# Kernel optimization log

Measured on AMD Instinct MI355X. Metric: run time of the kernel, lower is better.

The kernel has to match this reference:

```python
import jax, jax.numpy as jnp
import numpy as np

N_GROUP = 8
N_ITER = 3


def setup_inputs() -> dict:
    key = jax.random.key(0)
    x = jax.random.normal(key, (16, 64, 64, 512), dtype=jnp.float32)
    return {"x": x}


def reference(x):
    # x: [B, H, W, G*C] NHWC feature map
    B, H, W, Cg = x.shape
    G = N_GROUP
    C = Cg // G
    xr = x.reshape(B, H, W, G, C)  # [B,H,W,G,C]
    # routing logits per (batch, group); broadcastable against xr
    beta = jnp.zeros((B, 1, 1, G, 1), dtype=x.dtype)
    v = jnp.zeros((B, H, W, 1, C), dtype=x.dtype)
    for i in range(N_ITER):
        alpha = jax.nn.sigmoid(beta)                      # [B,1,1,G,1]
        v = jnp.sum(alpha * xr, axis=-2, keepdims=True)   # [B,H,W,1,C]
        if i < N_ITER - 1:
            # agreement: reduce over spatial dims and channels -> per (batch, group)
            beta = beta + jnp.sum(v * xr, axis=(1, 2, 4), keepdims=True)
    return v[..., 0, :]  # [B,H,W,C]
```

## Files before the change

### kernel.cpp

```cpp
#include <hip/hip_runtime.h>
#include <math.h>

#define BATCH   16
#define HW      4096
#define CG      512
#define NPAIR   36
#define F4_PER_POS   128
#define F4_PER_GROUP 16
#define SLOTS_PER_B  65536
#define XB_F4        524288

__global__ __launch_bounds__(256) void gram_kernel(const float* __restrict__ xf,
                                                   float* __restrict__ S) {
    const float4* x = (const float4*)xf;
    const int b = blockIdx.y;
    const int stride = gridDim.x * 256;
    int t = blockIdx.x * 256 + threadIdx.x;

    float acc[NPAIR];
#pragma unroll
    for (int p = 0; p < NPAIR; ++p) acc[p] = 0.f;

    const float4* xb = x + (long)b * XB_F4;
    for (int slot = t; slot < SLOTS_PER_B; slot += stride) {
        const int pos = slot >> 4;
        const int c4  = slot & 15;
        const float4* ptr = xb + pos * F4_PER_POS + c4;
        float4 xg[8];
#pragma unroll
        for (int g = 0; g < 8; ++g) xg[g] = ptr[g * F4_PER_GROUP];
        int p = 0;
#pragma unroll
        for (int g = 0; g < 8; ++g) {
#pragma unroll
            for (int gp = g; gp < 8; ++gp, ++p) {
                acc[p] += xg[g].x * xg[gp].x + xg[g].y * xg[gp].y +
                          xg[g].z * xg[gp].z + xg[g].w * xg[gp].w;
            }
        }
    }

#pragma unroll
    for (int p = 0; p < NPAIR; ++p) {
        float v = acc[p];
#pragma unroll
        for (int off = 32; off; off >>= 1) v += __shfl_xor(v, off, 64);
        acc[p] = v;
    }

    __shared__ float red[4][NPAIR];
    const int lane = threadIdx.x & 63;
    const int wave = threadIdx.x >> 6;
    if (lane == 0) {
#pragma unroll
        for (int p = 0; p < NPAIR; ++p) red[wave][p] = acc[p];
    }
    __syncthreads();
    if (threadIdx.x < NPAIR) {
        float v = red[0][threadIdx.x] + red[1][threadIdx.x] +
                  red[2][threadIdx.x] + red[3][threadIdx.x];
        atomicAdd(&S[b * NPAIR + threadIdx.x], v);
    }
}

__global__ __launch_bounds__(256) void out_kernel(const float* __restrict__ xf,
                                                  const float* __restrict__ S,
                                                  float* __restrict__ outf) {
    const float4* x = (const float4*)xf;
    float4* out = (float4*)outf;
    const int b   = blockIdx.x >> 8;
    const int blk = blockIdx.x & 255;

    __shared__ float alpha1s[8];
    __shared__ float alpha2s[8];

    const int g = threadIdx.x;
    float row[8];
    float beta1 = 0.f;
    if (g < 8) {
#pragma unroll
        for (int gp = 0; gp < 8; ++gp) {
            const int a  = g < gp ? g : gp;
            const int bb = g < gp ? gp : g;
            const int idx = a * 8 - (a * (a - 1)) / 2 + (bb - a);
            row[gp] = S[b * NPAIR + idx];
            beta1 += row[gp];
        }
        beta1 *= 0.5f;
        alpha1s[g] = 1.f / (1.f + expf(-beta1));
    }
    __syncthreads();
    if (g < 8) {
        float beta2 = beta1;
#pragma unroll
        for (int gp = 0; gp < 8; ++gp) beta2 += alpha1s[gp] * row[gp];
        alpha2s[g] = 1.f / (1.f + expf(-beta2));
    }
    __syncthreads();

    float a[8];
#pragma unroll
    for (int gg = 0; gg < 8; ++gg) a[gg] = alpha2s[gg];

    const int t   = blk * 256 + threadIdx.x;
    const int pos = t >> 4;
    const int c4  = t & 15;
    const float4* ptr = x + (long)b * XB_F4 + pos * F4_PER_POS + c4;

    float4 accv = make_float4(0.f, 0.f, 0.f, 0.f);
#pragma unroll
    for (int gg = 0; gg < 8; ++gg) {
        const float4 v = ptr[gg * F4_PER_GROUP];
        accv.x += a[gg] * v.x;
        accv.y += a[gg] * v.y;
        accv.z += a[gg] * v.z;
        accv.w += a[gg] * v.w;
    }
    out[(long)b * SLOTS_PER_B + t] = accv;
}

extern "C" void kernel_launch(void* const* d_in, const int* in_sizes, int n_in,
                              void* d_out, int out_size, void* d_ws, size_t ws_size,
                              hipStream_t stream) {
    const float* x = (const float*)d_in[0];
    float* out = (float*)d_out;
    float* S = (float*)d_ws;

    hipMemsetAsync(S, 0, BATCH * NPAIR * sizeof(float), stream);

    dim3 g1(64, BATCH);
    gram_kernel<<<g1, 256, 0, stream>>>(x, S);
    out_kernel<<<BATCH * 256, 256, 0, stream>>>(x, S, out);
}
```

Measured before the change: 217.2 us.

## Replace atomics and memset with per-block partials reduced in the output kernel

The Gram kernel now writes per-block partial sums to a workspace instead of atomically accumulating, which removes the hipMemsetAsync launch. The output kernel reduces the 64 partials per batch itself. The output kernel also processes 4 slots per thread with 4x fewer blocks and uses nontemporal stores. The cost is a redundant partial reduction in every output block and fewer blocks in flight.

```diff
diff --git a/kernel.cpp b/kernel.cpp
--- a/kernel.cpp
+++ b/kernel.cpp
@@ -3,26 +3,31 @@
 
 #define BATCH   16
 #define HW      4096
-#define CG      512
 #define NPAIR   36
 #define F4_PER_POS   128
 #define F4_PER_GROUP 16
 #define SLOTS_PER_B  65536
 #define XB_F4        524288
+#define BLOCKS_PER_BATCH 64
+#define NBLOCKS (BATCH * BLOCKS_PER_BATCH)
 
-__global__ __launch_bounds__(256) void gram_kernel(const float* __restrict__ xf,
-                                                   float* __restrict__ S) {
+typedef float f4v __attribute__((ext_vector_type(4)));
+
+__global__ __launch_bounds__(256) void gram_partial_kernel(
+    const float* __restrict__ xf, float* __restrict__ P) {
     const float4* x = (const float4*)xf;
-    const int b = blockIdx.y;
-    const int stride = gridDim.x * 256;
-    int t = blockIdx.x * 256 + threadIdx.x;
+    const int tid = threadIdx.x;
+    const int b   = blockIdx.x >> 6;
+    const int blk = blockIdx.x & 63;
+    const float4* xb = x + (long)b * XB_F4;
 
     float acc[NPAIR];
 #pragma unroll
     for (int p = 0; p < NPAIR; ++p) acc[p] = 0.f;
 
-    const float4* xb = x + (long)b * XB_F4;
-    for (int slot = t; slot < SLOTS_PER_B; slot += stride) {
+    int slot = blk * 256 + tid;
+#pragma unroll
+    for (int it = 0; it < 4; ++it, slot += BLOCKS_PER_BATCH * 256) {
         const int pos = slot >> 4;
         const int c4  = slot & 15;
         const float4* ptr = xb + pos * F4_PER_POS + c4;
@@ -49,74 +54,94 @@
     }
 
     __shared__ float red[4][NPAIR];
-    const int lane = threadIdx.x & 63;
-    const int wave = threadIdx.x >> 6;
+    const int lane = tid & 63;
+    const int wave = tid >> 6;
     if (lane == 0) {
 #pragma unroll
         for (int p = 0; p < NPAIR; ++p) red[wave][p] = acc[p];
     }
     __syncthreads();
-    if (threadIdx.x < NPAIR) {
-        float v = red[0][threadIdx.x] + red[1][threadIdx.x] +
-                  red[2][threadIdx.x] + red[3][threadIdx.x];
-        atomicAdd(&S[b * NPAIR + threadIdx.x], v);
+    if (tid < NPAIR) {
+        P[blockIdx.x * NPAIR + tid] =
+            red[0][tid] + red[1][tid] + red[2][tid] + red[3][tid];
     }
 }
 
-__global__ __launch_bounds__(256) void out_kernel(const float* __restrict__ xf,
-                                                  const float* __restrict__ S,
-                                                  float* __restrict__ outf) {
+__global__ __launch_bounds__(256) void out_kernel(
+    const float* __restrict__ xf, const float* __restrict__ P,
+    float* __restrict__ outf) {
     const float4* x = (const float4*)xf;
     float4* out = (float4*)outf;
-    const int b   = blockIdx.x >> 8;
-    const int blk = blockIdx.x & 255;
+    const int tid = threadIdx.x;
+    const int b   = blockIdx.x >> 6;
+    const int blk = blockIdx.x & 63;
+    const float4* xb = x + (long)b * XB_F4;
 
+    __shared__ float Sred[NPAIR][4];
+    __shared__ float S36[NPAIR];
     __shared__ float alpha1s[8];
     __shared__ float alpha2s[8];
 
-    const int g = threadIdx.x;
+    if (tid < NPAIR * 4) {
+        const int p = tid >> 2;
+        const int j = tid & 3;
+        float v = 0.f;
+#pragma unroll
+        for (int k = 0; k < 16; ++k)
+            v += P[(b * 64 + j * 16 + k) * NPAIR + p];
+        Sred[p][j] = v;
+    }
+    __syncthreads();
+    if (tid < NPAIR)
+        S36[tid] = Sred[tid][0] + Sred[tid][1] + Sred[tid][2] + Sred[tid][3];
+    __syncthreads();
+
     float row[8];
     float beta1 = 0.f;
-    if (g < 8) {
+    if (tid < 8) {
+        const int g = tid;
 #pragma unroll
         for (int gp = 0; gp < 8; ++gp) {
             const int a  = g < gp ? g : gp;
             const int bb = g < gp ? gp : g;
-            const int idx = a * 8 - (a * (a - 1)) / 2 + (bb - a);
-            row[gp] = S[b * NPAIR + idx];
+            row[gp] = S36[a * 8 - (a * (a - 1)) / 2 + (bb - a)];
             beta1 += row[gp];
         }
         beta1 *= 0.5f;
-        alpha1s[g] = 1.f / (1.f + expf(-beta1));
+        alpha1s[tid] = 1.f / (1.f + expf(-beta1));
     }
     __syncthreads();
-    if (g < 8) {
+    if (tid < 8) {
         float beta2 = beta1;
 #pragma unroll
         for (int gp = 0; gp < 8; ++gp) beta2 += alpha1s[gp] * row[gp];
-        alpha2s[g] = 1.f / (1.f + expf(-beta2));
+        alpha2s[tid] = 1.f / (1.f + expf(-beta2));
     }
     __syncthreads();
 
     float a[8];
 #pragma unroll
-    for (int gg = 0; gg < 8; ++gg) a[gg] = alpha2s[gg];
+    for (int g = 0; g < 8; ++g) a[g] = alpha2s[g];
 
-    const int t   = blk * 256 + threadIdx.x;
-    const int pos = t >> 4;
-    const int c4  = t & 15;
-    const float4* ptr = x + (long)b * XB_F4 + pos * F4_PER_POS + c4;
-
-    float4 accv = make_float4(0.f, 0.f, 0.f, 0.f);
+    const long obase = (long)b * SLOTS_PER_B;
 #pragma unroll
-    for (int gg = 0; gg < 8; ++gg) {
-        const float4 v = ptr[gg * F4_PER_GROUP];
-        accv.x += a[gg] * v.x;
-        accv.y += a[gg] * v.y;
-        accv.z += a[gg] * v.z;
-        accv.w += a[gg] * v.w;
+    for (int i = 0; i < 4; ++i) {
+        const int oslot = blk * 1024 + i * 256 + tid;
+        const int pos = oslot >> 4;
+        const int c4  = oslot & 15;
+        const float4* ptr = xb + pos * F4_PER_POS + c4;
+        float4 r = make_float4(0.f, 0.f, 0.f, 0.f);
+#pragma unroll
+        for (int g = 0; g < 8; ++g) {
+            const float4 v = ptr[g * F4_PER_GROUP];
+            r.x += a[g] * v.x;
+            r.y += a[g] * v.y;
+            r.z += a[g] * v.z;
+            r.w += a[g] * v.w;
+        }
+        f4v rv = {r.x, r.y, r.z, r.w};
+        __builtin_nontemporal_store(rv, (f4v*)&out[obase + oslot]);
     }
-    out[(long)b * SLOTS_PER_B + t] = accv;
 }
 
 extern "C" void kernel_launch(void* const* d_in, const int* in_sizes, int n_in,
@@ -124,11 +149,8 @@
                               hipStream_t stream) {
     const float* x = (const float*)d_in[0];
     float* out = (float*)d_out;
-    float* S = (float*)d_ws;
+    float* P = (float*)d_ws;
 
-    hipMemsetAsync(S, 0, BATCH * NPAIR * sizeof(float), stream);
-
-    dim3 g1(64, BATCH);
-    gram_kernel<<<g1, 256, 0, stream>>>(x, S);
-    out_kernel<<<BATCH * 256, 256, 0, stream>>>(x, S, out);
+    gram_partial_kernel<<<NBLOCKS, 256, 0, stream>>>(x, P);
+    out_kernel<<<NBLOCKS, 256, 0, stream>>>(x, P, out);
 }
```

New measurement: 216.0 us. Within noise of the previous version (-0.5%).
